# Optimization experiments

Measured on AMD Instinct MI355X. Metric: run time of the kernel, lower is better.

Reference implementation:

```python
import jax, jax.numpy as jnp
import numpy as np

NUM_GRAPHS = 2048
D_IN, D_H1, D_H2 = 1536, 64, 32


def setup_inputs() -> dict:
    key = jax.random.key(0)
    ks = jax.random.split(key, 8)
    features = jax.random.normal(ks[0], (131072, D_IN), dtype=jnp.float32)
    batch = jnp.sort(jax.random.randint(ks[1], (131072,), 0, NUM_GRAPHS, dtype=jnp.int64))
    # MLP params (Linear: y = x @ W.T + b), kaiming-ish scale
    W1 = jax.random.normal(ks[2], (D_H1, D_IN), dtype=jnp.float32) * (1.0 / np.sqrt(D_IN))
    b1 = jnp.zeros((D_H1,), dtype=jnp.float32)
    W2 = jax.random.normal(ks[3], (D_H2, D_H1), dtype=jnp.float32) * (1.0 / np.sqrt(D_H1))
    b2 = jnp.zeros((D_H2,), dtype=jnp.float32)
    W3 = jax.random.normal(ks[4], (1, D_H2), dtype=jnp.float32) * (1.0 / np.sqrt(D_H2))
    b3 = jnp.zeros((1,), dtype=jnp.float32)
    return {"features": features, "batch": batch, "W1": W1, "b1": b1,
            "W2": W2, "b2": b2, "W3": W3, "b3": b3}


def reference(features, batch, W1, b1, W2, b2, W3, b3):
    # Vectorized per-graph mean pooling (empty graphs -> zero features,
    # matching the torch branch that feeds zeros to the classifier).
    sums = jax.ops.segment_sum(features, batch, num_segments=NUM_GRAPHS)  # [G, D]
    counts = jax.ops.segment_sum(jnp.ones((features.shape[0],), features.dtype),
                                 batch, num_segments=NUM_GRAPHS)          # [G]
    means = sums / jnp.maximum(counts, 1.0)[:, None]                      # [G, D]
    # Tiny MLP classifier (dropout is identity in eval mode)
    h = jax.nn.relu(means @ W1.T + b1)
    h = jax.nn.relu(h @ W2.T + b2)
    out = h @ W3.T + b3                                                   # [G, 1]
    return out[:, 0]                                                      # [G]
```

## Files before the change

### kernel.cpp

```cpp
#include <hip/hip_runtime.h>

#define NGRAPHS 2048
#define DIN     1536
#define DH1     64
#define DH2     32

__global__ void find_offsets_kernel(const int* __restrict__ batch, int n,
                                    int* __restrict__ offsets) {
    int i = blockIdx.x * blockDim.x + threadIdx.x;
    if (i >= n) return;
    int b = batch[i];
    int prev = (i == 0) ? -1 : batch[i - 1];
    for (int g = prev + 1; g <= b; ++g) offsets[g] = i;
    if (i == n - 1) {
        for (int g = b + 1; g <= NGRAPHS; ++g) offsets[g] = n;
    }
}

__global__ __launch_bounds__(384) void pool_mlp_kernel(
    const float* __restrict__ features,
    const int* __restrict__ offsets,
    const float* __restrict__ W1, const float* __restrict__ b1,
    const float* __restrict__ W2, const float* __restrict__ b2,
    const float* __restrict__ W3, const float* __restrict__ b3,
    float* __restrict__ out)
{
    const int g    = blockIdx.x;
    const int tid  = threadIdx.x;
    const int lane = tid & 63;
    const int wave = tid >> 6;

    const int s = offsets[g];
    const int e = offsets[g + 1];

    __shared__ float mean_s[DIN];
    __shared__ float h1_s[DH1];
    __shared__ float h2_s[DH2];

    const float4* __restrict__ F4 = reinterpret_cast<const float4*>(features);
    float4 a0 = make_float4(0.f, 0.f, 0.f, 0.f);
    float4 a1 = make_float4(0.f, 0.f, 0.f, 0.f);
    float4 a2 = make_float4(0.f, 0.f, 0.f, 0.f);
    float4 a3 = make_float4(0.f, 0.f, 0.f, 0.f);

    int r = s;
    for (; r + 4 <= e; r += 4) {
        float4 v0 = F4[(size_t)(r + 0) * (DIN / 4) + tid];
        float4 v1 = F4[(size_t)(r + 1) * (DIN / 4) + tid];
        float4 v2 = F4[(size_t)(r + 2) * (DIN / 4) + tid];
        float4 v3 = F4[(size_t)(r + 3) * (DIN / 4) + tid];
        a0.x += v0.x; a0.y += v0.y; a0.z += v0.z; a0.w += v0.w;
        a1.x += v1.x; a1.y += v1.y; a1.z += v1.z; a1.w += v1.w;
        a2.x += v2.x; a2.y += v2.y; a2.z += v2.z; a2.w += v2.w;
        a3.x += v3.x; a3.y += v3.y; a3.z += v3.z; a3.w += v3.w;
    }
    for (; r < e; ++r) {
        float4 v = F4[(size_t)r * (DIN / 4) + tid];
        a0.x += v.x; a0.y += v.y; a0.z += v.z; a0.w += v.w;
    }
    a0.x += a1.x + a2.x + a3.x;
    a0.y += a1.y + a2.y + a3.y;
    a0.z += a1.z + a2.z + a3.z;
    a0.w += a1.w + a2.w + a3.w;

    const int cnt = e - s;
    const float inv = 1.0f / (float)(cnt > 1 ? cnt : 1);
    a0.x *= inv; a0.y *= inv; a0.z *= inv; a0.w *= inv;
    reinterpret_cast<float4*>(mean_s)[tid] = a0;
    __syncthreads();

    const float4* __restrict__ m4 = reinterpret_cast<const float4*>(mean_s);
    for (int j = wave; j < DH1; j += 6) {
        const float4* __restrict__ w4 =
            reinterpret_cast<const float4*>(W1 + (size_t)j * DIN);
        float acc = 0.f;
        #pragma unroll
        for (int k = 0; k < DIN / 4 / 64; ++k) {
            float4 w = w4[k * 64 + lane];
            float4 m = m4[k * 64 + lane];
            acc += m.x * w.x + m.y * w.y + m.z * w.z + m.w * w.w;
        }
        #pragma unroll
        for (int off = 32; off; off >>= 1) acc += __shfl_xor(acc, off, 64);
        if (lane == 0) h1_s[j] = fmaxf(acc + b1[j], 0.f);
    }
    __syncthreads();

    for (int j = wave; j < DH2; j += 6) {
        float acc = h1_s[lane] * W2[(size_t)j * DH1 + lane];
        #pragma unroll
        for (int off = 32; off; off >>= 1) acc += __shfl_xor(acc, off, 64);
        if (lane == 0) h2_s[j] = fmaxf(acc + b2[j], 0.f);
    }
    __syncthreads();

    if (wave == 0) {
        float acc = (lane < DH2) ? h2_s[lane] * W3[lane] : 0.f;
        #pragma unroll
        for (int off = 32; off; off >>= 1) acc += __shfl_xor(acc, off, 64);
        if (lane == 0) out[g] = acc + b3[0];
    }
}

extern "C" void kernel_launch(void* const* d_in, const int* in_sizes, int n_in,
                              void* d_out, int out_size, void* d_ws, size_t ws_size,
                              hipStream_t stream) {
    const float* features = (const float*)d_in[0];
    const int*   batch    = (const int*)d_in[1];
    const float* W1 = (const float*)d_in[2];
    const float* b1 = (const float*)d_in[3];
    const float* W2 = (const float*)d_in[4];
    const float* b2 = (const float*)d_in[5];
    const float* W3 = (const float*)d_in[6];
    const float* b3 = (const float*)d_in[7];
    float* out = (float*)d_out;

    const int n = in_sizes[1];
    int* offsets = (int*)d_ws;

    find_offsets_kernel<<<(n + 255) / 256, 256, 0, stream>>>(batch, n, offsets);
    pool_mlp_kernel<<<NGRAPHS, 384, 0, stream>>>(features, offsets,
                                                 W1, b1, W2, b2, W3, b3, out);
}
```

Before: 176.6 us.

## Split pooling and MLP into separate kernels with batched MLP over graphs

Separates mean pooling into its own kernel that writes per-graph means to workspace, then runs a batched MLP kernel handling 8 graphs per block so W1 rows are reused across graphs. The goal is to remove the per-graph W1 re-read and the MLP tail that stalls each pooling block. In exchange it adds an extra launch plus a write and re-read of the 12 MB means buffer. A fused fallback path is kept for when the workspace is too small.

```diff
diff --git a/kernel.cpp b/kernel.cpp
--- a/kernel.cpp
+++ b/kernel.cpp
@@ -4,6 +4,7 @@
 #define DIN     1536
 #define DH1     64
 #define DH2     32
+#define MLPG    8
 
 __global__ void find_offsets_kernel(const int* __restrict__ batch, int n,
                                     int* __restrict__ offsets) {
@@ -17,7 +18,105 @@
     }
 }
 
-__global__ __launch_bounds__(384) void pool_mlp_kernel(
+__global__ __launch_bounds__(384) void pool_kernel(
+    const float* __restrict__ features,
+    const int* __restrict__ offsets,
+    float* __restrict__ means)
+{
+    const int g   = blockIdx.x;
+    const int tid = threadIdx.x;
+    const int s   = offsets[g];
+    const int e   = offsets[g + 1];
+
+    const float4* __restrict__ F4 = reinterpret_cast<const float4*>(features);
+    float4 a0 = make_float4(0.f, 0.f, 0.f, 0.f);
+    float4 a1 = make_float4(0.f, 0.f, 0.f, 0.f);
+    float4 a2 = make_float4(0.f, 0.f, 0.f, 0.f);
+    float4 a3 = make_float4(0.f, 0.f, 0.f, 0.f);
+
+    int r = s;
+    for (; r + 4 <= e; r += 4) {
+        float4 v0 = F4[(size_t)(r + 0) * (DIN / 4) + tid];
+        float4 v1 = F4[(size_t)(r + 1) * (DIN / 4) + tid];
+        float4 v2 = F4[(size_t)(r + 2) * (DIN / 4) + tid];
+        float4 v3 = F4[(size_t)(r + 3) * (DIN / 4) + tid];
+        a0.x += v0.x; a0.y += v0.y; a0.z += v0.z; a0.w += v0.w;
+        a1.x += v1.x; a1.y += v1.y; a1.z += v1.z; a1.w += v1.w;
+        a2.x += v2.x; a2.y += v2.y; a2.z += v2.z; a2.w += v2.w;
+        a3.x += v3.x; a3.y += v3.y; a3.z += v3.z; a3.w += v3.w;
+    }
+    for (; r < e; ++r) {
+        float4 v = F4[(size_t)r * (DIN / 4) + tid];
+        a0.x += v.x; a0.y += v.y; a0.z += v.z; a0.w += v.w;
+    }
+    a0.x += a1.x + a2.x + a3.x;
+    a0.y += a1.y + a2.y + a3.y;
+    a0.z += a1.z + a2.z + a3.z;
+    a0.w += a1.w + a2.w + a3.w;
+
+    const int cnt = e - s;
+    const float inv = 1.0f / (float)(cnt > 1 ? cnt : 1);
+    a0.x *= inv; a0.y *= inv; a0.z *= inv; a0.w *= inv;
+    reinterpret_cast<float4*>(means)[(size_t)g * (DIN / 4) + tid] = a0;
+}
+
+__global__ __launch_bounds__(256) void mlp_kernel(
+    const float* __restrict__ means,
+    const float* __restrict__ W1, const float* __restrict__ b1,
+    const float* __restrict__ W2, const float* __restrict__ b2,
+    const float* __restrict__ W3, const float* __restrict__ b3,
+    float* __restrict__ out)
+{
+    const int tid  = threadIdx.x;
+    const int lane = tid & 63;
+    const int bg   = blockIdx.x * MLPG;
+
+    __shared__ float h1_s[MLPG][DH1];
+    __shared__ float h2_s[MLPG][DH2];
+
+    {
+        const int g0 = __builtin_amdgcn_readfirstlane((tid >> 6) * 2);
+        const float4* __restrict__ m0 =
+            reinterpret_cast<const float4*>(means + (size_t)(bg + g0) * DIN);
+        const float4* __restrict__ m1 =
+            reinterpret_cast<const float4*>(means + (size_t)(bg + g0 + 1) * DIN);
+        const float4* __restrict__ w1r =
+            reinterpret_cast<const float4*>(W1 + (size_t)lane * DIN);
+        float a0 = 0.f, a1 = 0.f;
+        #pragma unroll 8
+        for (int k = 0; k < DIN / 4; ++k) {
+            float4 wv = w1r[k];
+            float4 u  = m0[k];
+            float4 v  = m1[k];
+            a0 += wv.x * u.x + wv.y * u.y + wv.z * u.z + wv.w * u.w;
+            a1 += wv.x * v.x + wv.y * v.y + wv.z * v.z + wv.w * v.w;
+        }
+        const float bb = b1[lane];
+        h1_s[g0 + 0][lane] = fmaxf(a0 + bb, 0.f);
+        h1_s[g0 + 1][lane] = fmaxf(a1 + bb, 0.f);
+    }
+    __syncthreads();
+
+    {
+        const int g = tid >> 5;
+        const int j = tid & 31;
+        const float* __restrict__ w2r = W2 + (size_t)j * DH1;
+        float a = b2[j];
+        #pragma unroll
+        for (int k = 0; k < DH1; ++k) a += h1_s[g][k] * w2r[k];
+        h2_s[g][j] = fmaxf(a, 0.f);
+    }
+    __syncthreads();
+
+    if (tid < MLPG) {
+        float a = b3[0];
+        #pragma unroll
+        for (int j = 0; j < DH2; ++j) a += h2_s[tid][j] * W3[j];
+        out[bg + tid] = a;
+    }
+}
+
+__global__ __launch_bounds__(384) void pool_mlp_fused_kernel(
     const float* __restrict__ features,
     const int* __restrict__ offsets,
     const float* __restrict__ W1, const float* __restrict__ b1,
@@ -39,30 +138,10 @@
 
     const float4* __restrict__ F4 = reinterpret_cast<const float4*>(features);
     float4 a0 = make_float4(0.f, 0.f, 0.f, 0.f);
-    float4 a1 = make_float4(0.f, 0.f, 0.f, 0.f);
-    float4 a2 = make_float4(0.f, 0.f, 0.f, 0.f);
-    float4 a3 = make_float4(0.f, 0.f, 0.f, 0.f);
-
-    int r = s;
-    for (; r + 4 <= e; r += 4) {
-        float4 v0 = F4[(size_t)(r + 0) * (DIN / 4) + tid];
-        float4 v1 = F4[(size_t)(r + 1) * (DIN / 4) + tid];
-        float4 v2 = F4[(size_t)(r + 2) * (DIN / 4) + tid];
-        float4 v3 = F4[(size_t)(r + 3) * (DIN / 4) + tid];
-        a0.x += v0.x; a0.y += v0.y; a0.z += v0.z; a0.w += v0.w;
-        a1.x += v1.x; a1.y += v1.y; a1.z += v1.z; a1.w += v1.w;
-        a2.x += v2.x; a2.y += v2.y; a2.z += v2.z; a2.w += v2.w;
-        a3.x += v3.x; a3.y += v3.y; a3.z += v3.z; a3.w += v3.w;
-    }
-    for (; r < e; ++r) {
+    for (int r = s; r < e; ++r) {
         float4 v = F4[(size_t)r * (DIN / 4) + tid];
         a0.x += v.x; a0.y += v.y; a0.z += v.z; a0.w += v.w;
     }
-    a0.x += a1.x + a2.x + a3.x;
-    a0.y += a1.y + a2.y + a3.y;
-    a0.z += a1.z + a2.z + a3.z;
-    a0.w += a1.w + a2.w + a3.w;
-
     const int cnt = e - s;
     const float inv = 1.0f / (float)(cnt > 1 ? cnt : 1);
     a0.x *= inv; a0.y *= inv; a0.z *= inv; a0.w *= inv;
@@ -117,8 +196,18 @@
 
     const int n = in_sizes[1];
     int* offsets = (int*)d_ws;
+    const size_t means_off = 16384;
+    float* means = (float*)((char*)d_ws + means_off);
+    const size_t need = means_off + (size_t)NGRAPHS * DIN * sizeof(float);
 
     find_offsets_kernel<<<(n + 255) / 256, 256, 0, stream>>>(batch, n, offsets);
-    pool_mlp_kernel<<<NGRAPHS, 384, 0, stream>>>(features, offsets,
-                                                 W1, b1, W2, b2, W3, b3, out);
-}
+
+    if (ws_size >= need) {
+        pool_kernel<<<NGRAPHS, 384, 0, stream>>>(features, offsets, means);
+        mlp_kernel<<<NGRAPHS / MLPG, 256, 0, stream>>>(means, W1, b1, W2, b2,
+                                                       W3, b3, out);
+    } else {
+        pool_mlp_fused_kernel<<<NGRAPHS, 384, 0, stream>>>(features, offsets,
+                                                           W1, b1, W2, b2, W3, b3, out);
+    }
+}
```

Result: slower. 216.2 us (+22.5%).

## Use persistent blocks with atomic work-stealing over graphs and nontemporal feature loads

Applied to the files above, without the earlier changes.

Replaces the one-block-per-graph launch with 1280 persistent blocks that claim graphs through a global atomic counter. The counter is reset inside the offsets kernel. Feature rows are read with nontemporal loads and accumulated with native vector types. The aim is to balance uneven graph sizes across CUs, cut block launch overhead, and keep streamed features from polluting the cache, at the cost of an atomic plus an extra barrier per graph.

```diff
diff --git a/kernel.cpp b/kernel.cpp
--- a/kernel.cpp
+++ b/kernel.cpp
@@ -4,10 +4,15 @@
 #define DIN     1536
 #define DH1     64
 #define DH2     32
+#define POOL_BLOCKS 1280
+
+typedef float fvec4 __attribute__((ext_vector_type(4)));
 
 __global__ void find_offsets_kernel(const int* __restrict__ batch, int n,
-                                    int* __restrict__ offsets) {
+                                    int* __restrict__ offsets,
+                                    int* __restrict__ counter) {
     int i = blockIdx.x * blockDim.x + threadIdx.x;
+    if (i == 0) *counter = 0;
     if (i >= n) return;
     int b = batch[i];
     int prev = (i == 0) ? -1 : batch[i - 1];
@@ -17,88 +22,91 @@
     }
 }
 
-__global__ __launch_bounds__(384) void pool_mlp_kernel(
+__global__ __launch_bounds__(384) void pool_mlp_ws_kernel(
     const float* __restrict__ features,
     const int* __restrict__ offsets,
     const float* __restrict__ W1, const float* __restrict__ b1,
     const float* __restrict__ W2, const float* __restrict__ b2,
     const float* __restrict__ W3, const float* __restrict__ b3,
-    float* __restrict__ out)
+    float* __restrict__ out,
+    int* __restrict__ counter)
 {
-    const int g    = blockIdx.x;
     const int tid  = threadIdx.x;
     const int lane = tid & 63;
     const int wave = tid >> 6;
 
-    const int s = offsets[g];
-    const int e = offsets[g + 1];
-
     __shared__ float mean_s[DIN];
     __shared__ float h1_s[DH1];
     __shared__ float h2_s[DH2];
+    __shared__ int   g_s;
 
-    const float4* __restrict__ F4 = reinterpret_cast<const float4*>(features);
-    float4 a0 = make_float4(0.f, 0.f, 0.f, 0.f);
-    float4 a1 = make_float4(0.f, 0.f, 0.f, 0.f);
-    float4 a2 = make_float4(0.f, 0.f, 0.f, 0.f);
-    float4 a3 = make_float4(0.f, 0.f, 0.f, 0.f);
+    const fvec4* __restrict__ F4 = reinterpret_cast<const fvec4*>(features);
 
-    int r = s;
-    for (; r + 4 <= e; r += 4) {
-        float4 v0 = F4[(size_t)(r + 0) * (DIN / 4) + tid];
-        float4 v1 = F4[(size_t)(r + 1) * (DIN / 4) + tid];
-        float4 v2 = F4[(size_t)(r + 2) * (DIN / 4) + tid];
-        float4 v3 = F4[(size_t)(r + 3) * (DIN / 4) + tid];
-        a0.x += v0.x; a0.y += v0.y; a0.z += v0.z; a0.w += v0.w;
-        a1.x += v1.x; a1.y += v1.y; a1.z += v1.z; a1.w += v1.w;
-        a2.x += v2.x; a2.y += v2.y; a2.z += v2.z; a2.w += v2.w;
-        a3.x += v3.x; a3.y += v3.y; a3.z += v3.z; a3.w += v3.w;
-    }
-    for (; r < e; ++r) {
-        float4 v = F4[(size_t)r * (DIN / 4) + tid];
-        a0.x += v.x; a0.y += v.y; a0.z += v.z; a0.w += v.w;
-    }
-    a0.x += a1.x + a2.x + a3.x;
-    a0.y += a1.y + a2.y + a3.y;
-    a0.z += a1.z + a2.z + a3.z;
-    a0.w += a1.w + a2.w + a3.w;
+    for (;;) {
+        if (tid == 0) g_s = atomicAdd(counter, 1);
+        __syncthreads();
+        const int g = g_s;
+        if (g >= NGRAPHS) break;
 
-    const int cnt = e - s;
-    const float inv = 1.0f / (float)(cnt > 1 ? cnt : 1);
-    a0.x *= inv; a0.y *= inv; a0.z *= inv; a0.w *= inv;
-    reinterpret_cast<float4*>(mean_s)[tid] = a0;
-    __syncthreads();
+        const int s = offsets[g];
+        const int e = offsets[g + 1];
 
-    const float4* __restrict__ m4 = reinterpret_cast<const float4*>(mean_s);
-    for (int j = wave; j < DH1; j += 6) {
-        const float4* __restrict__ w4 =
-            reinterpret_cast<const float4*>(W1 + (size_t)j * DIN);
-        float acc = 0.f;
-        #pragma unroll
-        for (int k = 0; k < DIN / 4 / 64; ++k) {
-            float4 w = w4[k * 64 + lane];
-            float4 m = m4[k * 64 + lane];
-            acc += m.x * w.x + m.y * w.y + m.z * w.z + m.w * w.w;
+        fvec4 a0 = (fvec4)(0.f);
+        fvec4 a1 = (fvec4)(0.f);
+        fvec4 a2 = (fvec4)(0.f);
+        fvec4 a3 = (fvec4)(0.f);
+        int r = s;
+        for (; r + 4 <= e; r += 4) {
+            fvec4 v0 = __builtin_nontemporal_load(&F4[(size_t)(r + 0) * (DIN / 4) + tid]);
+            fvec4 v1 = __builtin_nontemporal_load(&F4[(size_t)(r + 1) * (DIN / 4) + tid]);
+            fvec4 v2 = __builtin_nontemporal_load(&F4[(size_t)(r + 2) * (DIN / 4) + tid]);
+            fvec4 v3 = __builtin_nontemporal_load(&F4[(size_t)(r + 3) * (DIN / 4) + tid]);
+            a0 += v0; a1 += v1; a2 += v2; a3 += v3;
         }
-        #pragma unroll
-        for (int off = 32; off; off >>= 1) acc += __shfl_xor(acc, off, 64);
-        if (lane == 0) h1_s[j] = fmaxf(acc + b1[j], 0.f);
-    }
-    __syncthreads();
+        for (; r < e; ++r) {
+            fvec4 v = __builtin_nontemporal_load(&F4[(size_t)r * (DIN / 4) + tid]);
+            a0 += v;
+        }
+        a0 += a1 + a2 + a3;
 
-    for (int j = wave; j < DH2; j += 6) {
-        float acc = h1_s[lane] * W2[(size_t)j * DH1 + lane];
-        #pragma unroll
-        for (int off = 32; off; off >>= 1) acc += __shfl_xor(acc, off, 64);
-        if (lane == 0) h2_s[j] = fmaxf(acc + b2[j], 0.f);
-    }
-    __syncthreads();
+        const int cnt = e - s;
+        const float inv = 1.0f / (float)(cnt > 1 ? cnt : 1);
+        a0 *= inv;
+        reinterpret_cast<fvec4*>(mean_s)[tid] = a0;
+        __syncthreads();
 
-    if (wave == 0) {
-        float acc = (lane < DH2) ? h2_s[lane] * W3[lane] : 0.f;
-        #pragma unroll
-        for (int off = 32; off; off >>= 1) acc += __shfl_xor(acc, off, 64);
-        if (lane == 0) out[g] = acc + b3[0];
+        const fvec4* __restrict__ m4 = reinterpret_cast<const fvec4*>(mean_s);
+        for (int j = wave; j < DH1; j += 6) {
+            const fvec4* __restrict__ w4 =
+                reinterpret_cast<const fvec4*>(W1 + (size_t)j * DIN);
+            float acc = 0.f;
+            #pragma unroll
+            for (int k = 0; k < DIN / 4 / 64; ++k) {
+                fvec4 w = w4[k * 64 + lane];
+                fvec4 m = m4[k * 64 + lane];
+                acc += m.x * w.x + m.y * w.y + m.z * w.z + m.w * w.w;
+            }
+            #pragma unroll
+            for (int off = 32; off; off >>= 1) acc += __shfl_xor(acc, off, 64);
+            if (lane == 0) h1_s[j] = fmaxf(acc + b1[j], 0.f);
+        }
+        __syncthreads();
+
+        for (int j = wave; j < DH2; j += 6) {
+            float acc = h1_s[lane] * W2[(size_t)j * DH1 + lane];
+            #pragma unroll
+            for (int off = 32; off; off >>= 1) acc += __shfl_xor(acc, off, 64);
+            if (lane == 0) h2_s[j] = fmaxf(acc + b2[j], 0.f);
+        }
+        __syncthreads();
+
+        if (wave == 0) {
+            float acc = (lane < DH2) ? h2_s[lane] * W3[lane] : 0.f;
+            #pragma unroll
+            for (int off = 32; off; off >>= 1) acc += __shfl_xor(acc, off, 64);
+            if (lane == 0) out[g] = acc + b3[0];
+        }
+        __syncthreads();
     }
 }
 
@@ -116,9 +124,12 @@
     float* out = (float*)d_out;
 
     const int n = in_sizes[1];
-    int* offsets = (int*)d_ws;
+    int* counter = (int*)d_ws;
+    int* offsets = (int*)d_ws + 64;
 
-    find_offsets_kernel<<<(n + 255) / 256, 256, 0, stream>>>(batch, n, offsets);
-    pool_mlp_kernel<<<NGRAPHS, 384, 0, stream>>>(features, offsets,
-                                                 W1, b1, W2, b2, W3, b3, out);
+    find_offsets_kernel<<<(n + 255) / 256, 256, 0, stream>>>(batch, n, offsets,
+                                                             counter);
+    pool_mlp_ws_kernel<<<POOL_BLOCKS, 384, 0, stream>>>(features, offsets,
+                                                        W1, b1, W2, b2, W3, b3,
+                                                        out, counter);
 }
```

Result: faster. 163.4 us (-7.5%).
